# Optimization experiments

Measured on AMD Instinct MI355X. Metric: run time of the kernel, lower is better.

## Reference

```python
import jax, jax.numpy as jnp
import numpy as np

B, T, D = 4, 2048, 1024
H, S = 16, 64  # n_heads, stalk_dim; D == H*S
P_ADIC_BASE = 2
MAX_VAL = 16


def quantize_6bit(x):
    # symmetric int6 quantization with straight-through estimator
    scale = jnp.max(jnp.abs(x)) / 31.0 + 1e-8
    q = jnp.clip(jnp.round(x / scale), -31, 31) * scale
    return x + jax.lax.stop_gradient(q - x)


def build_p_adic_bias(seq_len, p=2, max_val=16):
    idx = jnp.arange(seq_len)
    d = jnp.abs(idx[:, None] - idx[None, :])
    nonzero = d > 0
    vp = jnp.zeros_like(d)
    work = d
    for _ in range(max_val):  # fixed iterations; v_2(|i-j|) <= log2(T) < 16
        divisible = nonzero & (work % p == 0)
        vp = vp + divisible.astype(vp.dtype)
        work = jnp.where(divisible, work // p, work)
    vals = jnp.minimum(vp, max_val).astype(jnp.float32)
    vals = jnp.where(nonzero, vals, jnp.float32(max_val))
    return vals / max_val


def setup_inputs() -> dict:
    key = jax.random.key(0)
    ks = jax.random.split(key, 8)
    std = 0.02
    return {
        "x": jax.random.normal(ks[0], (B, T, D), dtype=jnp.float32),
        "wq": jax.random.normal(ks[1], (D, D), dtype=jnp.float32) * std,
        "wk": jax.random.normal(ks[2], (D, D), dtype=jnp.float32) * std,
        "wv": jax.random.normal(ks[3], (D, D), dtype=jnp.float32) * std,
        "wo": jax.random.normal(ks[4], (D, D), dtype=jnp.float32) * std,
        "wu": jax.random.normal(ks[5], (S, S), dtype=jnp.float32) * std,
        "wsv": jax.random.normal(ks[6], (S, S), dtype=jnp.float32) * std,
        "p_scale": jnp.ones((1,), dtype=jnp.float32) * 0.1,
    }


def reference(x, wq, wk, wv, wo, wu, wsv, p_scale):
    h, s = H, S
    scale = 1.0 / jnp.sqrt(jnp.float32(s))
    # quantized linear projections (F.linear: x @ W.T)
    Q = (x @ quantize_6bit(wq).T).reshape(B, T, h, s).transpose(0, 2, 1, 3)
    K = (x @ quantize_6bit(wk).T).reshape(B, T, h, s).transpose(0, 2, 1, 3)
    V = (x @ quantize_6bit(wv).T).reshape(B, T, h, s).transpose(0, 2, 1, 3)
    # stalk (low-rank sheaf) maps on the head dim
    Qs = Q @ quantize_6bit(wu).T
    Ks = K @ quantize_6bit(wsv).T
    scores = jnp.einsum("bhqs,bhks->bhqk", Qs, Ks) * scale
    p_bias = build_p_adic_bias(T, p=P_ADIC_BASE, max_val=MAX_VAL)
    scores = scores + p_scale[0] * p_bias[None, None, :, :]
    causal = jnp.triu(jnp.ones((T, T), dtype=bool), k=1)
    scores = jnp.where(causal[None, None], -jnp.inf, scores)
    attn = jax.nn.softmax(scores, axis=-1)
    out = jnp.einsum("bhqk,bhks->bhqs", attn, V)
    out = out.transpose(0, 2, 1, 3).reshape(B, T, D)
    return out @ quantize_6bit(wo).T
```

## Files before the change

### kernel.cpp

```cpp
#include <hip/hip_runtime.h>
#include <hip/hip_bf16.h>
#include <stdint.h>


typedef __bf16 bf16_t;
typedef __attribute__((ext_vector_type(4))) __bf16 bf16x4;
typedef __attribute__((ext_vector_type(8))) __bf16 bf16x8;
typedef __attribute__((ext_vector_type(4))) float f32x4;

#define BB 4
#define TT 2048
#define DD 1024
#define HH 16
#define SS 64

__device__ __forceinline__ float quant6(float v, float s) {
    float q = rintf(v / s);
    q = fminf(fmaxf(q, -31.0f), 31.0f);
    return q * s;
}

__device__ __forceinline__ float fexp2(float x) {
#if __has_builtin(__builtin_amdgcn_exp2f)
    return __builtin_amdgcn_exp2f(x);
#else
    return exp2f(x);
#endif
}

typedef __attribute__((address_space(3))) uint32_t lds_u32;
typedef const __attribute__((address_space(1))) uint32_t glb_u32;

__global__ __launch_bounds__(256) void absmax6(const float* __restrict__ wq,
                                               const float* __restrict__ wk,
                                               const float* __restrict__ wv,
                                               const float* __restrict__ wo,
                                               const float* __restrict__ wu,
                                               const float* __restrict__ wsv,
                                               float* __restrict__ amax) {
    const int t = blockIdx.y;
    const float* src = (t == 0) ? wq : (t == 1) ? wk : (t == 2) ? wv
                     : (t == 3) ? wo : (t == 4) ? wu : wsv;
    const int n4 = (t < 4) ? (1048576 / 4) : (4096 / 4);
    float m = 0.0f;
    for (int i = blockIdx.x * blockDim.x + threadIdx.x; i < n4; i += gridDim.x * blockDim.x) {
        float4 v = ((const float4*)src)[i];
        m = fmaxf(m, fmaxf(fmaxf(fabsf(v.x), fabsf(v.y)), fmaxf(fabsf(v.z), fabsf(v.w))));
    }
    #pragma unroll
    for (int mask = 32; mask > 0; mask >>= 1)
        m = fmaxf(m, __shfl_xor(m, mask));
    __shared__ float red[4];
    int w = threadIdx.x >> 6;
    if ((threadIdx.x & 63) == 0) red[w] = m;
    __syncthreads();
    if (threadIdx.x == 0) {
        m = fmaxf(fmaxf(red[0], red[1]), fmaxf(red[2], red[3]));
        atomicMax((int*)(amax + t), __float_as_int(m));
    }
}

__global__ __launch_bounds__(256) void xcvt_kernel(const float* __restrict__ x,
                                                   bf16_t* __restrict__ xb) {
    int i = (blockIdx.x * 256 + threadIdx.x) * 8;
    float4 f0 = *(const float4*)(x + i);
    float4 f1 = *(const float4*)(x + i + 4);
    bf16x8 v;
    v[0] = (bf16_t)f0.x; v[1] = (bf16_t)f0.y; v[2] = (bf16_t)f0.z; v[3] = (bf16_t)f0.w;
    v[4] = (bf16_t)f1.x; v[5] = (bf16_t)f1.y; v[6] = (bf16_t)f1.z; v[7] = (bf16_t)f1.w;
    *(bf16x8*)(xb + i) = v;
}

__global__ __launch_bounds__(256) void prep_w(const float* __restrict__ wq,
                                              const float* __restrict__ wk,
                                              const float* __restrict__ wv,
                                              const float* __restrict__ wo,
                                              const float* __restrict__ wu,
                                              const float* __restrict__ wsv,
                                              const float* __restrict__ amax,
                                              bf16_t* __restrict__ W_all,
                                              bf16_t* __restrict__ Wo) {
    const int which = blockIdx.y;
    if (blockIdx.x < 512) {
        const float* src = which ? wo : wv;
        bf16_t* dst = which ? Wo : (W_all + (size_t)2048 * 1024);
        float s = amax[which ? 3 : 2] / 31.0f + 1e-8f;
        int i = (blockIdx.x * 256 + threadIdx.x) * 8;
        float4 f0 = *(const float4*)(src + i);
        float4 f1 = *(const float4*)(src + i + 4);
        bf16x8 v;
        v[0] = (bf16_t)quant6(f0.x, s); v[1] = (bf16_t)quant6(f0.y, s);
        v[2] = (bf16_t)quant6(f0.z, s); v[3] = (bf16_t)quant6(f0.w, s);
        v[4] = (bf16_t)quant6(f1.x, s); v[5] = (bf16_t)quant6(f1.y, s);
        v[6] = (bf16_t)quant6(f1.z, s); v[7] = (bf16_t)quant6(f1.w, s);
        *(bf16x8*)(dst + i) = v;
        return;
    }
    const int fx = blockIdx.x - 512;
    const float* wbig = which ? wk : wq;
    const float* wsml = which ? wsv : wu;
    const float sb = amax[which ? 1 : 0] / 31.0f + 1e-8f;
    const float ss = amax[which ? 5 : 4] / 31.0f + 1e-8f;
    const float oscale = which ? 1.0f : 0.125f * 1.44269504089f;
    bf16_t* outp = W_all + (size_t)which * 1024 * 1024;
    const int h = fx >> 4, n0 = (fx & 15) * 64;
    const int w = threadIdx.x >> 6, l = threadIdx.x & 63;
    const int l15 = l & 15, quad = l >> 4, q8 = quad * 8;
    const int m0 = w * 16;

    bf16x8 af[2];
    #pragma unroll
    for (int kc = 0; kc < 2; ++kc) {
        const float* src = wsml + (m0 + l15) * 64 + kc * 32 + q8;
        float4 f0 = *(const float4*)(src);
        float4 f1 = *(const float4*)(src + 4);
        bf16x8 a;
        a[0] = (bf16_t)quant6(f0.x, ss); a[1] = (bf16_t)quant6(f0.y, ss);
        a[2] = (bf16_t)quant6(f0.z, ss); a[3] = (bf16_t)quant6(f0.w, ss);
        a[4] = (bf16_t)quant6(f1.x, ss); a[5] = (bf16_t)quant6(f1.y, ss);
        a[6] = (bf16_t)quant6(f1.z, ss); a[7] = (bf16_t)quant6(f1.w, ss);
        af[kc] = a;
    }
    f32x4 acc[4];
    #pragma unroll
    for (int nb = 0; nb < 4; ++nb) acc[nb] = (f32x4){0.f, 0.f, 0.f, 0.f};
    #pragma unroll
    for (int kc = 0; kc < 2; ++kc) {
        #pragma unroll
        for (int nb = 0; nb < 4; ++nb) {
            bf16x8 bfr;
            #pragma unroll
            for (int j = 0; j < 8; ++j)
                bfr[j] = (bf16_t)quant6(wbig[(size_t)(h * 64 + kc * 32 + q8 + j) * 1024 + n0 + nb * 16 + l15], sb);
            acc[nb] = __builtin_amdgcn_mfma_f32_16x16x32_bf16(af[kc], bfr, acc[nb], 0, 0, 0);
        }
    }
    #pragma unroll
    for (int nb = 0; nb < 4; ++nb)
        #pragma unroll
        for (int r = 0; r < 4; ++r)
            outp[(size_t)(h * 64 + m0 + quad * 4 + r) * 1024 + n0 + nb * 16 + l15] =
                (bf16_t)(acc[nb][r] * oscale);
}

template <bool OUT_F32>
__global__ __launch_bounds__(256) void gemm128(const bf16_t* __restrict__ A,
                                               const bf16_t* __restrict__ Bt,
                                               void* __restrict__ Cv,
                                               int lda, int ldb, int ldc, int K) {
    __shared__ __align__(16) bf16_t As[128 * 64];
    __shared__ __align__(16) bf16_t Bs[128 * 64];
    const int tid = threadIdx.x;
    const int w = tid >> 6, l = tid & 63;
    const int l15 = l & 15, quad = l >> 4;
    const int m0 = blockIdx.y * 128, n0 = blockIdx.x * 128;
    const int wm = (w & 1) * 64, wn = (w >> 1) * 64;

    f32x4 acc[4][4];
    #pragma unroll
    for (int a = 0; a < 4; ++a)
        #pragma unroll
        for (int b = 0; b < 4; ++b) acc[a][b] = (f32x4){0.f, 0.f, 0.f, 0.f};

    for (int kc = 0; kc < K; kc += 64) {
        __syncthreads();
        #pragma unroll
        for (int rep = 0; rep < 4; ++rep) {
            int ci = rep * 256 + w * 64 + l;
            int row = ci >> 3, slot = ci & 7;
            int gch = slot ^ ((row ^ (row >> 3)) & 7);
            __builtin_amdgcn_global_load_lds(
                (glb_u32*)(A + (size_t)(m0 + row) * lda + kc + gch * 8),
                (lds_u32*)(As + (rep * 256 + w * 64) * 8), 16, 0, 0);
            __builtin_amdgcn_global_load_lds(
                (glb_u32*)(Bt + (size_t)(n0 + row) * ldb + kc + gch * 8),
                (lds_u32*)(Bs + (rep * 256 + w * 64) * 8), 16, 0, 0);
        }
        __syncthreads();
        #pragma unroll
        for (int kb = 0; kb < 2; ++kb) {
            bf16x8 af[4], bfr[4];
            #pragma unroll
            for (int mb = 0; mb < 4; ++mb) {
                int row = wm + mb * 16 + l15;
                int slot = ((kb << 2) + quad) ^ ((row ^ (row >> 3)) & 7);
                af[mb] = *(const bf16x8*)(As + (row << 6) + slot * 8);
            }
            #pragma unroll
            for (int nb = 0; nb < 4; ++nb) {
                int row = wn + nb * 16 + l15;
                int slot = ((kb << 2) + quad) ^ ((row ^ (row >> 3)) & 7);
                bfr[nb] = *(const bf16x8*)(Bs + (row << 6) + slot * 8);
            }
            #pragma unroll
            for (int mb = 0; mb < 4; ++mb)
                #pragma unroll
                for (int nb = 0; nb < 4; ++nb)
                    acc[mb][nb] = __builtin_amdgcn_mfma_f32_16x16x32_bf16(af[mb], bfr[nb], acc[mb][nb], 0, 0, 0);
        }
    }
    #pragma unroll
    for (int mb = 0; mb < 4; ++mb) {
        #pragma unroll
        for (int nb = 0; nb < 4; ++nb) {
            int col = n0 + wn + nb * 16 + l15;
            #pragma unroll
            for (int r = 0; r < 4; ++r) {
                int row = m0 + wm + mb * 16 + quad * 4 + r;
                if constexpr (OUT_F32)
                    ((float*)Cv)[(size_t)row * ldc + col] = acc[mb][nb][r];
                else
                    ((bf16_t*)Cv)[(size_t)row * ldc + col] = (bf16_t)acc[mb][nb][r];
            }
        }
    }
}

__global__ __launch_bounds__(256) void vtrans_kernel(const bf16_t* __restrict__ QKV,
                                                     bf16_t* __restrict__ Vt) {
    __shared__ __align__(16) bf16_t tile[64 * 72];
    const int tid = threadIdx.x;
    const int bh = blockIdx.x >> 5, tt = blockIdx.x & 31;
    const int b = bh >> 4, h = bh & 15;
    #pragma unroll
    for (int rep = 0; rep < 2; ++rep) {
        int ci = rep * 256 + tid;
        int row = ci >> 3, ch = ci & 7;
        bf16x8 v = *(const bf16x8*)(QKV + ((size_t)(b * TT + tt * 64 + row)) * 3072 + 2048 + h * 64 + ch * 8);
        #pragma unroll
        for (int j = 0; j < 8; ++j) tile[(ch * 8 + j) * 72 + row] = v[j];
    }
    __syncthreads();
    #pragma unroll
    for (int rep = 0; rep < 2; ++rep) {
        int ci = rep * 256 + tid;
        int s = ci >> 3, ch = ci & 7;
        bf16x8 v = *(const bf16x8*)(tile + s * 72 + ch * 8);
        *(bf16x8*)(Vt + ((size_t)(bh * 64 + s)) * TT + tt * 64 + ch * 8) = v;
    }
}

__device__ __forceinline__ void attn_step(bf16_t* __restrict__ Pw,
                                          const bf16x8 kb[4][2], const bf16x8 vb[4][2],
                                          const bf16x8 qa[2],
                                          f32x4* oacc, float& lrun,
                                          int qlane, int kbase, bool diag, float pb2,
                                          int l15, int quad) {
    f32x4 sacc[4];
    #pragma unroll
    for (int c = 0; c < 4; ++c) sacc[c] = (f32x4){0.f, 0.f, 0.f, 0.f};
    #pragma unroll
    for (int kc = 0; kc < 2; ++kc)
        #pragma unroll
        for (int c = 0; c < 4; ++c)
            sacc[c] = __builtin_amdgcn_mfma_f32_16x16x32_bf16(kb[c][kc], qa[kc], sacc[c], 0, 0, 0);

    const int kp0 = kbase + quad * 4;
    #pragma unroll
    for (int c = 0; c < 4; ++c) {
        bf16x4 pk;
        #pragma unroll
        for (int r = 0; r < 4; ++r) {
            const int k = kp0 + c * 16 + r;
            const int d = qlane - k;
            float ctzf = (float)__builtin_ctz((unsigned)d | 0x10000u);
            float s2 = sacc[c][r] + pb2 * ctzf;
            if (diag && k > qlane) s2 = -INFINITY;
            float p = fexp2(s2);
            lrun += p;
            pk[r] = (bf16_t)p;
        }
        int pp = (c * 2 + (quad >> 1)) ^ (l15 & 7);
        *(bf16x4*)(Pw + l15 * 64 + pp * 8 + (quad & 1) * 4) = pk;
    }
    __builtin_amdgcn_wave_barrier();
    #pragma unroll
    for (int kc = 0; kc < 2; ++kc) {
        bf16x8 pa = *(const bf16x8*)(Pw + l15 * 64 + (((kc * 4 + quad) ^ (l15 & 7)) * 8));
        #pragma unroll
        for (int sb = 0; sb < 4; ++sb)
            oacc[sb] = __builtin_amdgcn_mfma_f32_16x16x32_bf16(pa, vb[sb][kc], oacc[sb], 0, 0, 0);
    }
    __builtin_amdgcn_wave_barrier();
}

__global__ __launch_bounds__(256, 2) void attn_kernel(const bf16_t* __restrict__ QKV,
                                                      const bf16_t* __restrict__ Vt,
                                                      const float* __restrict__ p_scale_ptr,
                                                      bf16_t* __restrict__ O) {
    __shared__ __align__(16) bf16_t Ks[64 * 64];
    __shared__ __align__(16) bf16_t Vs[64 * 64];
    __shared__ __align__(16) bf16_t Ps[4 * 16 * 64];

    const int tid = threadIdx.x;
    const int w = tid >> 6, l = tid & 63;
    const int l15 = l & 15, quad = l >> 4, q8 = quad * 8;
    const int pair = (blockIdx.x >> 3) & 15;
    const int bh = (blockIdx.x & 7) + ((blockIdx.x >> 7) << 3);
    const int b = bh >> 4, h = bh & 15;
    const int qtA = pair, qtB = 31 - pair;
    const int q0A = qtA * 64 + w * 16, q0B = qtB * 64 + w * 16;
    const int qlA = q0A + l15, qlB = q0B + l15;

    const float pb2 = p_scale_ptr[0] * 1.44269504089f * 0.0625f;
    const size_t xbase = (size_t)b * TT * 3072;

    bf16x8 qaA[2], qaB[2];
    #pragma unroll
    for (int kc = 0; kc < 2; ++kc) {
        qaA[kc] = *(const bf16x8*)(QKV + xbase + (size_t)(q0A + l15) * 3072 + h * 64 + kc * 32 + q8);
        qaB[kc] = *(const bf16x8*)(QKV + xbase + (size_t)(q0B + l15) * 3072 + h * 64 + kc * 32 + q8);
    }

    f32x4 oA[4], oB[4];
    float lA = 0.f, lB = 0.f;
    #pragma unroll
    for (int i = 0; i < 4; ++i) {
        oA[i] = (f32x4){0.f, 0.f, 0.f, 0.f};
        oB[i] = (f32x4){0.f, 0.f, 0.f, 0.f};
    }
    bf16_t* Pw = Ps + w * 1024;

    for (int kt = 0; kt <= qtB; ++kt) {
        const int kbase = kt * 64;
        __syncthreads();
        #pragma unroll
        for (int rep = 0; rep < 2; ++rep) {
            int ci = rep * 256 + tid;
            int row = ci >> 3, slot = ci & 7;
            int gch = slot ^ ((row ^ (row >> 3)) & 7);
            __builtin_amdgcn_global_load_lds(
                (glb_u32*)(QKV + xbase + (size_t)(kbase + row) * 3072 + 1024 + h * 64 + gch * 8),
                (lds_u32*)(Ks + (rep * 256 + w * 64) * 8), 16, 0, 0);
            __builtin_amdgcn_global_load_lds(
                (glb_u32*)(Vt + (size_t)bh * 131072 + (size_t)row * 2048 + kbase + gch * 8),
                (lds_u32*)(Vs + (rep * 256 + w * 64) * 8), 16, 0, 0);
        }
        __syncthreads();
        bf16x8 kb[4][2], vb[4][2];
        #pragma unroll
        for (int kc = 0; kc < 2; ++kc) {
            #pragma unroll
            for (int c = 0; c < 4; ++c) {
                int row = c * 16 + l15;
                int slot = (kc * 4 + quad) ^ ((row ^ (row >> 3)) & 7);
                kb[c][kc] = *(const bf16x8*)(Ks + row * 64 + slot * 8);
                vb[c][kc] = *(const bf16x8*)(Vs + row * 64 + slot * 8);
            }
        }
        attn_step(Pw, kb, vb, qaB, oB, lB, qlB, kbase, kt == qtB, pb2, l15, quad);
        if (kt <= qtA)
            attn_step(Pw, kb, vb, qaA, oA, lA, qlA, kbase, kt == qtA, pb2, l15, quad);
    }

    #pragma unroll
    for (int t = 0; t < 2; ++t) {
        float s = t ? lB : lA;
        f32x4* oo = t ? oB : oA;
        int q0 = t ? q0B : q0A;
        s += __shfl_xor(s, 16);
        s += __shfl_xor(s, 32);
        float inv = 1.0f / s;
        #pragma unroll
        for (int r = 0; r < 4; ++r) {
            float invr = __shfl(inv, quad * 4 + r);
            #pragma unroll
            for (int sb = 0; sb < 4; ++sb) {
                int q = q0 + quad * 4 + r;
                int col = h * 64 + sb * 16 + l15;
                O[(size_t)(b * TT + q) * DD + col] = (bf16_t)(oo[sb][r] * invr);
            }
        }
    }
}

extern "C" void kernel_launch(void* const* d_in, const int* in_sizes, int n_in,
                              void* d_out, int out_size, void* d_ws, size_t ws_size,
                              hipStream_t stream) {
    const float* x   = (const float*)d_in[0];
    const float* wq  = (const float*)d_in[1];
    const float* wk  = (const float*)d_in[2];
    const float* wv  = (const float*)d_in[3];
    const float* wo  = (const float*)d_in[4];
    const float* wu  = (const float*)d_in[5];
    const float* wsv = (const float*)d_in[6];
    const float* psc = (const float*)d_in[7];
    float* out = (float*)d_out;

    char* ws = (char*)d_ws;
    float*  amax  = (float*)(ws);
    bf16_t* W_all = (bf16_t*)(ws + 256);
    bf16_t* Wo    = (bf16_t*)(ws + 6291712);
    bf16_t* xb    = (bf16_t*)(ws + 8388864);
    bf16_t* Obuf  = xb;
    bf16_t* QKV   = (bf16_t*)(ws + 25166080);
    bf16_t* Vt    = (bf16_t*)(ws + 75497728);

    hipLaunchKernelGGL(absmax6, dim3(64, 6), dim3(256), 0, stream, wq, wk, wv, wo, wu, wsv, amax);
    hipLaunchKernelGGL(prep_w, dim3(768, 2), dim3(256), 0, stream,
                       wq, wk, wv, wo, wu, wsv, amax, W_all, Wo);
    hipLaunchKernelGGL(xcvt_kernel, dim3(4096), dim3(256), 0, stream, x, xb);

    hipLaunchKernelGGL((gemm128<false>), dim3(24, 64), dim3(256), 0, stream,
                       xb, W_all, (void*)QKV, 1024, 1024, 3072, 1024);

    hipLaunchKernelGGL(vtrans_kernel, dim3(2048), dim3(256), 0, stream, QKV, Vt);

    hipLaunchKernelGGL(attn_kernel, dim3(1024), dim3(256), 0, stream, QKV, Vt, psc, Obuf);

    hipLaunchKernelGGL((gemm128<true>), dim3(8, 64), dim3(256), 0, stream,
                       Obuf, Wo, (void*)out, 1024, 1024, 1024, 1024);
}
```

Measured before the change: 288.8 us.

## Double-buffer K/V LDS tiles and specialize attention step for diagonal tiles

Measured after the change: 288.8 us. About the same (-0.0%).

```diff
diff --git a/kernel.cpp b/kernel.cpp
--- a/kernel.cpp
+++ b/kernel.cpp
@@ -240,11 +240,12 @@
     }
 }
 
+template <bool DIAG>
 __device__ __forceinline__ void attn_step(bf16_t* __restrict__ Pw,
                                           const bf16x8 kb[4][2], const bf16x8 vb[4][2],
                                           const bf16x8 qa[2],
                                           f32x4* oacc, float& lrun,
-                                          int qlane, int kbase, bool diag, float pb2,
+                                          int qlane, int kbase, float pb2,
                                           int l15, int quad) {
     f32x4 sacc[4];
     #pragma unroll
@@ -263,9 +264,15 @@
         for (int r = 0; r < 4; ++r) {
             const int k = kp0 + c * 16 + r;
             const int d = qlane - k;
-            float ctzf = (float)__builtin_ctz((unsigned)d | 0x10000u);
-            float s2 = sacc[c][r] + pb2 * ctzf;
-            if (diag && k > qlane) s2 = -INFINITY;
+            float s2;
+            if constexpr (DIAG) {
+                float ctzf = (float)__builtin_ctz((unsigned)d | 0x10000u);
+                s2 = sacc[c][r] + pb2 * ctzf;
+                if (k > qlane) s2 = -INFINITY;
+            } else {
+                float ctzf = (float)__builtin_ctz((unsigned)d);
+                s2 = sacc[c][r] + pb2 * ctzf;
+            }
             float p = fexp2(s2);
             lrun += p;
             pk[r] = (bf16_t)p;
@@ -288,8 +295,8 @@
                                                       const bf16_t* __restrict__ Vt,
                                                       const float* __restrict__ p_scale_ptr,
                                                       bf16_t* __restrict__ O) {
-    __shared__ __align__(16) bf16_t Ks[64 * 64];
-    __shared__ __align__(16) bf16_t Vs[64 * 64];
+    __shared__ __align__(16) bf16_t Ks[2 * 64 * 64];
+    __shared__ __align__(16) bf16_t Vs[2 * 64 * 64];
     __shared__ __align__(16) bf16_t Ps[4 * 16 * 64];
 
     const int tid = threadIdx.x;
@@ -321,22 +328,29 @@
     }
     bf16_t* Pw = Ps + w * 1024;
 
-    for (int kt = 0; kt <= qtB; ++kt) {
-        const int kbase = kt * 64;
-        __syncthreads();
+    auto STAGE = [&](int kt2, int buf2) {
+        const int kb2 = kt2 * 64;
         #pragma unroll
         for (int rep = 0; rep < 2; ++rep) {
             int ci = rep * 256 + tid;
             int row = ci >> 3, slot = ci & 7;
             int gch = slot ^ ((row ^ (row >> 3)) & 7);
             __builtin_amdgcn_global_load_lds(
-                (glb_u32*)(QKV + xbase + (size_t)(kbase + row) * 3072 + 1024 + h * 64 + gch * 8),
-                (lds_u32*)(Ks + (rep * 256 + w * 64) * 8), 16, 0, 0);
+                (glb_u32*)(QKV + xbase + (size_t)(kb2 + row) * 3072 + 1024 + h * 64 + gch * 8),
+                (lds_u32*)(Ks + buf2 * 4096 + (rep * 256 + w * 64) * 8), 16, 0, 0);
             __builtin_amdgcn_global_load_lds(
-                (glb_u32*)(Vt + (size_t)bh * 131072 + (size_t)row * 2048 + kbase + gch * 8),
-                (lds_u32*)(Vs + (rep * 256 + w * 64) * 8), 16, 0, 0);
-        }
+                (glb_u32*)(Vt + (size_t)bh * 131072 + (size_t)row * 2048 + kb2 + gch * 8),
+                (lds_u32*)(Vs + buf2 * 4096 + (rep * 256 + w * 64) * 8), 16, 0, 0);
+        }
+    };
+
+    const int nkt = qtB + 1;
+    STAGE(0, 0);
+    for (int kt = 0; kt < nkt; ++kt) {
+        const int kbase = kt * 64;
+        const int buf = kt & 1;
         __syncthreads();
+        if (kt + 1 < nkt) STAGE(kt + 1, buf ^ 1);
         bf16x8 kb[4][2], vb[4][2];
         #pragma unroll
         for (int kc = 0; kc < 2; ++kc) {
@@ -344,13 +358,20 @@
             for (int c = 0; c < 4; ++c) {
                 int row = c * 16 + l15;
                 int slot = (kc * 4 + quad) ^ ((row ^ (row >> 3)) & 7);
-                kb[c][kc] = *(const bf16x8*)(Ks + row * 64 + slot * 8);
-                vb[c][kc] = *(const bf16x8*)(Vs + row * 64 + slot * 8);
-            }
-        }
-        attn_step(Pw, kb, vb, qaB, oB, lB, qlB, kbase, kt == qtB, pb2, l15, quad);
-        if (kt <= qtA)
-            attn_step(Pw, kb, vb, qaA, oA, lA, qlA, kbase, kt == qtA, pb2, l15, quad);
+                kb[c][kc] = *(const bf16x8*)(Ks + buf * 4096 + row * 64 + slot * 8);
+                vb[c][kc] = *(const bf16x8*)(Vs + buf * 4096 + row * 64 + slot * 8);
+            }
+        }
+        if (kt == qtB)
+            attn_step<true>(Pw, kb, vb, qaB, oB, lB, qlB, kbase, pb2, l15, quad);
+        else
+            attn_step<false>(Pw, kb, vb, qaB, oB, lB, qlB, kbase, pb2, l15, quad);
+        if (kt <= qtA) {
+            if (kt == qtA)
+                attn_step<true>(Pw, kb, vb, qaA, oA, lA, qlA, kbase, pb2, l15, quad);
+            else
+                attn_step<false>(Pw, kb, vb, qaA, oA, lA, qlA, kbase, pb2, l15, quad);
+        }
     }
 
     #pragma unroll
```

## Precompute p-adic bias/mask table and compute softmax row sums via MFMA

Applied to the files above, without the earlier changes.

Measured after the change: 280.5 us. 2.9% less time.

```diff
diff --git a/kernel.cpp b/kernel.cpp
--- a/kernel.cpp
+++ b/kernel.cpp
@@ -30,6 +30,25 @@
 
 typedef __attribute__((address_space(3))) uint32_t lds_u32;
 typedef const __attribute__((address_space(1))) uint32_t glb_u32;
+
+__global__ __launch_bounds__(256) void ptable_kernel(const float* __restrict__ psc,
+                                                     float* __restrict__ tbl) {
+    const int idx = blockIdx.x * 256 + threadIdx.x;
+    const int l = idx & 63, c = (idx >> 6) & 3, e = idx >> 8;
+    const int l15 = l & 15, quad = l >> 4;
+    const float pb2 = psc[0] * 1.44269504089f * 0.0625f;
+    f32x4 v;
+    #pragma unroll
+    for (int r = 0; r < 4; ++r) {
+        const int d = e * 16 + l15 - (c * 16 + quad * 4 + r);
+        float val;
+        if (d < 0) val = -INFINITY;
+        else if (d == 0) val = pb2 * 16.0f;
+        else val = pb2 * (float)__builtin_ctz((unsigned)d);
+        v[r] = val;
+    }
+    *(f32x4*)(tbl + (size_t)idx * 4) = v;
+}
 
 __global__ __launch_bounds__(256) void absmax6(const float* __restrict__ wq,
                                                const float* __restrict__ wk,
@@ -242,34 +261,25 @@
 
 __device__ __forceinline__ void attn_step(bf16_t* __restrict__ Pw,
                                           const bf16x8 kb[4][2], const bf16x8 vb[4][2],
-                                          const bf16x8 qa[2],
-                                          f32x4* oacc, float& lrun,
-                                          int qlane, int kbase, bool diag, float pb2,
+                                          const bf16x8 qa[2], const bf16x8 ones,
+                                          const f32x4 binit[4],
+                                          f32x4* oacc, f32x4& lacc,
                                           int l15, int quad) {
     f32x4 sacc[4];
     #pragma unroll
-    for (int c = 0; c < 4; ++c) sacc[c] = (f32x4){0.f, 0.f, 0.f, 0.f};
+    for (int c = 0; c < 4; ++c) sacc[c] = binit[c];
     #pragma unroll
     for (int kc = 0; kc < 2; ++kc)
         #pragma unroll
         for (int c = 0; c < 4; ++c)
             sacc[c] = __builtin_amdgcn_mfma_f32_16x16x32_bf16(kb[c][kc], qa[kc], sacc[c], 0, 0, 0);
 
-    const int kp0 = kbase + quad * 4;
     #pragma unroll
     for (int c = 0; c < 4; ++c) {
         bf16x4 pk;
         #pragma unroll
-        for (int r = 0; r < 4; ++r) {
-            const int k = kp0 + c * 16 + r;
-            const int d = qlane - k;
-            float ctzf = (float)__builtin_ctz((unsigned)d | 0x10000u);
-            float s2 = sacc[c][r] + pb2 * ctzf;
-            if (diag && k > qlane) s2 = -INFINITY;
-            float p = fexp2(s2);
-            lrun += p;
-            pk[r] = (bf16_t)p;
-        }
+        for (int r = 0; r < 4; ++r)
+            pk[r] = (bf16_t)fexp2(sacc[c][r]);
         int pp = (c * 2 + (quad >> 1)) ^ (l15 & 7);
         *(bf16x4*)(Pw + l15 * 64 + pp * 8 + (quad & 1) * 4) = pk;
     }
@@ -280,13 +290,14 @@
         #pragma unroll
         for (int sb = 0; sb < 4; ++sb)
             oacc[sb] = __builtin_amdgcn_mfma_f32_16x16x32_bf16(pa, vb[sb][kc], oacc[sb], 0, 0, 0);
+        lacc = __builtin_amdgcn_mfma_f32_16x16x32_bf16(pa, ones, lacc, 0, 0, 0);
     }
     __builtin_amdgcn_wave_barrier();
 }
 
 __global__ __launch_bounds__(256, 2) void attn_kernel(const bf16_t* __restrict__ QKV,
                                                       const bf16_t* __restrict__ Vt,
-                                                      const float* __restrict__ p_scale_ptr,
+                                                      const float* __restrict__ Bias,
                                                       bf16_t* __restrict__ O) {
     __shared__ __align__(16) bf16_t Ks[64 * 64];
     __shared__ __align__(16) bf16_t Vs[64 * 64];
@@ -300,9 +311,7 @@
     const int b = bh >> 4, h = bh & 15;
     const int qtA = pair, qtB = 31 - pair;
     const int q0A = qtA * 64 + w * 16, q0B = qtB * 64 + w * 16;
-    const int qlA = q0A + l15, qlB = q0B + l15;
-
-    const float pb2 = p_scale_ptr[0] * 1.44269504089f * 0.0625f;
+
     const size_t xbase = (size_t)b * TT * 3072;
 
     bf16x8 qaA[2], qaB[2];
@@ -312,8 +321,13 @@
         qaB[kc] = *(const bf16x8*)(QKV + xbase + (size_t)(q0B + l15) * 3072 + h * 64 + kc * 32 + q8);
     }
 
-    f32x4 oA[4], oB[4];
-    float lA = 0.f, lB = 0.f;
+    bf16x8 ones;
+    #pragma unroll
+    for (int j = 0; j < 8; ++j) ones[j] = (bf16_t)1.0f;
+
+    f32x4 oA[4], oB[4], lA, lB;
+    lA = (f32x4){0.f, 0.f, 0.f, 0.f};
+    lB = (f32x4){0.f, 0.f, 0.f, 0.f};
     #pragma unroll
     for (int i = 0; i < 4; ++i) {
         oA[i] = (f32x4){0.f, 0.f, 0.f, 0.f};
@@ -321,8 +335,8 @@
     }
     bf16_t* Pw = Ps + w * 1024;
 
-    for (int kt = 0; kt <= qtB; ++kt) {
-        const int kbase = kt * 64;
+    const int nkt = qtB + 1;
+    for (int kt = 0; kt < nkt; ++kt) {
         __syncthreads();
         #pragma unroll
         for (int rep = 0; rep < 2; ++rep) {
@@ -330,11 +344,23 @@
             int row = ci >> 3, slot = ci & 7;
             int gch = slot ^ ((row ^ (row >> 3)) & 7);
             __builtin_amdgcn_global_load_lds(
-                (glb_u32*)(QKV + xbase + (size_t)(kbase + row) * 3072 + 1024 + h * 64 + gch * 8),
+                (glb_u32*)(QKV + xbase + (size_t)(kt * 64 + row) * 3072 + 1024 + h * 64 + gch * 8),
                 (lds_u32*)(Ks + (rep * 256 + w * 64) * 8), 16, 0, 0);
             __builtin_amdgcn_global_load_lds(
-                (glb_u32*)(Vt + (size_t)bh * 131072 + (size_t)row * 2048 + kbase + gch * 8),
+                (glb_u32*)(Vt + (size_t)bh * 131072 + (size_t)row * 2048 + kt * 64 + gch * 8),
                 (lds_u32*)(Vs + (rep * 256 + w * 64) * 8), 16, 0, 0);
+        }
+        const bool doA = kt <= qtA;
+        f32x4 bB[4], bA[4];
+        {
+            const float* bp = Bias + ((((size_t)(qtB - kt) * 4 + w) * 4) * 64 + l) * 4;
+            #pragma unroll
+            for (int c = 0; c < 4; ++c) bB[c] = *(const f32x4*)(bp + c * 256);
+        }
+        if (doA) {
+            const float* bp = Bias + ((((size_t)(qtA - kt) * 4 + w) * 4) * 64 + l) * 4;
+            #pragma unroll
+            for (int c = 0; c < 4; ++c) bA[c] = *(const f32x4*)(bp + c * 256);
         }
         __syncthreads();
         bf16x8 kb[4][2], vb[4][2];
@@ -348,22 +374,19 @@
                 vb[c][kc] = *(const bf16x8*)(Vs + row * 64 + slot * 8);
             }
         }
-        attn_step(Pw, kb, vb, qaB, oB, lB, qlB, kbase, kt == qtB, pb2, l15, quad);
-        if (kt <= qtA)
-            attn_step(Pw, kb, vb, qaA, oA, lA, qlA, kbase, kt == qtA, pb2, l15, quad);
+        attn_step(Pw, kb, vb, qaB, ones, bB, oB, lB, l15, quad);
+        if (doA)
+            attn_step(Pw, kb, vb, qaA, ones, bA, oA, lA, l15, quad);
     }
 
     #pragma unroll
     for (int t = 0; t < 2; ++t) {
-        float s = t ? lB : lA;
+        const f32x4 lc = t ? lB : lA;
         f32x4* oo = t ? oB : oA;
         int q0 = t ? q0B : q0A;
-        s += __shfl_xor(s, 16);
-        s += __shfl_xor(s, 32);
-        float inv = 1.0f / s;
         #pragma unroll
         for (int r = 0; r < 4; ++r) {
-            float invr = __shfl(inv, quad * 4 + r);
+            float invr = 1.0f / lc[r];
             #pragma unroll
             for (int sb = 0; sb < 4; ++sb) {
                 int q = q0 + quad * 4 + r;
@@ -395,7 +418,9 @@
     bf16_t* Obuf  = xb;
     bf16_t* QKV   = (bf16_t*)(ws + 25166080);
     bf16_t* Vt    = (bf16_t*)(ws + 75497728);
-
+    float*  Bias  = (float*)(ws + 92274944);
+
+    hipLaunchKernelGGL(ptable_kernel, dim3(128), dim3(256), 0, stream, psc, Bias);
     hipLaunchKernelGGL(absmax6, dim3(64, 6), dim3(256), 0, stream, wq, wk, wv, wo, wu, wsv, amax);
     hipLaunchKernelGGL(prep_w, dim3(768, 2), dim3(256), 0, stream,
                        wq, wk, wv, wo, wu, wsv, amax, W_all, Wo);
@@ -406,7 +431,7 @@
 
     hipLaunchKernelGGL(vtrans_kernel, dim3(2048), dim3(256), 0, stream, QKV, Vt);
 
-    hipLaunchKernelGGL(attn_kernel, dim3(1024), dim3(256), 0, stream, QKV, Vt, psc, Obuf);
+    hipLaunchKernelGGL(attn_kernel, dim3(1024), dim3(256), 0, stream, QKV, Vt, Bias, Obuf);
 
     hipLaunchKernelGGL((gemm128<true>), dim3(8, 64), dim3(256), 0, stream,
                        Obuf, Wo, (void*)out, 1024, 1024, 1024, 1024);
```
